# Kernel optimization log

Hardware: AMD Instinct MI355X
Metric: run time of the kernel (lower is better)

Reference implementation:

```python
import jax, jax.numpy as jnp
import numpy as np
from math import factorial

RS1 = [(16, 0), (8, 1), (4, 2)]
RS2 = [(16, 0), (8, 1), (4, 2)]


def _su2_cg(j1, j2, j3, m1, m2, m3):
    # Clebsch-Gordan coefficient <j1 m1 j2 m2 | j3 m3> (integer j's)
    if m3 != m1 + m2:
        return 0.0
    f = factorial
    vmin = int(max(-j1 + j2 + m3, -j1 + m1, 0))
    vmax = int(min(j2 + j3 + m1, j3 - j1 + j2, j3 + m3))
    C = ((2.0 * j3 + 1.0) * f(j3 + j1 - j2) * f(j3 - j1 + j2) * f(j1 + j2 - j3)
         * f(j3 + m3) * f(j3 - m3)
         / (f(j1 + j2 + j3 + 1) * f(j1 - m1) * f(j1 + m1) * f(j2 - m2) * f(j2 + m2))) ** 0.5
    S = 0.0
    for v in range(vmin, vmax + 1):
        S += (-1.0) ** (v + j2 + m2) * f(j2 + j3 + m1 - v) * f(j1 - m1 + v) \
             / (f(v) * f(j3 - j1 + j2 - v) * f(j3 + m3 - v) * f(v + j1 - j2 - m3))
    return C * S


def _su2_tensor(j1, j2, j3):
    C = np.zeros((2 * j1 + 1, 2 * j2 + 1, 2 * j3 + 1))
    for m1 in range(-j1, j1 + 1):
        for m2 in range(-j2, j2 + 1):
            m3 = m1 + m2
            if abs(m3) <= j3:
                C[m1 + j1, m2 + j2, m3 + j3] = _su2_cg(j1, j2, j3, m1, m2, m3)
    return C


def _change_basis_real_to_complex(l):
    q = np.zeros((2 * l + 1, 2 * l + 1), dtype=np.complex128)
    for m in range(-l, 0):
        q[l + m, l + abs(m)] = 2 ** -0.5
        q[l + m, l - abs(m)] = -1j * 2 ** -0.5
    q[l, l] = 1.0
    for m in range(1, l + 1):
        q[l + m, l + abs(m)] = (-1) ** m * 2 ** -0.5
        q[l + m, l - abs(m)] = 1j * (-1) ** m * 2 ** -0.5
    return ((-1j) ** l) * q


def _real_cg(l1, l2, l3):
    # CG tensor in the real spherical-harmonic basis, shape (2l1+1, 2l2+1, 2l3+1)
    C = _su2_tensor(l1, l2, l3)
    Q1 = _change_basis_real_to_complex(l1)
    Q2 = _change_basis_real_to_complex(l2)
    Q3 = _change_basis_real_to_complex(l3)
    C = np.einsum('ij,kl,mn,ikn->jlm', Q1, Q2, np.conj(Q3.T), C)
    return np.real(C)


def build_mixing_matrix(Rs1, Rs2):
    dim_in1 = sum(mul * (2 * l + 1) for mul, l in Rs1)
    dim_in2 = sum(mul * (2 * l + 1) for mul, l in Rs2)
    K = sum(m1 * m2 * (2 * l + 1)
            for m1, l1 in Rs1 for m2, l2 in Rs2
            for l in range(abs(l1 - l2), l1 + l2 + 1))
    M = np.zeros((K, dim_in1, dim_in2), dtype=np.float32)
    k_off = 0
    i_off = 0
    for mul1, l1 in Rs1:
        d1 = 2 * l1 + 1
        j_off = 0
        for mul2, l2 in Rs2:
            d2 = 2 * l2 + 1
            for l in range(abs(l1 - l2), l1 + l2 + 1):
                dl = 2 * l + 1
                # 'component' normalization
                C = (_real_cg(l1, l2, l) * (dl ** 0.5)).astype(np.float32)
                Ck = np.transpose(C, (2, 0, 1))  # (dl, d1, d2)
                for u in range(mul1):
                    for v in range(mul2):
                        k0 = k_off + (u * mul2 + v) * dl
                        M[k0:k0 + dl,
                          i_off + u * d1:i_off + (u + 1) * d1,
                          j_off + v * d2:j_off + (v + 1) * d2] = Ck
                k_off += mul1 * mul2 * dl
            j_off += mul2 * d2
        i_off += mul1 * d1
    return M


def setup_inputs() -> dict:
    key = jax.random.key(0)
    k1, k2 = jax.random.split(key)
    Z = 4096
    f1 = jax.random.normal(k1, (Z, 60), dtype=jnp.float32)
    f2 = jax.random.normal(k2, (Z, 60), dtype=jnp.float32)
    mix = jnp.asarray(build_mixing_matrix(RS1, RS2))  # (3600, 60, 60)
    return {"features_1": f1, "features_2": f2, "mixing_matrix": mix}


def reference(features_1, features_2, mixing_matrix):
    # output[z, k] = sum_{i,j} C[k,i,j] * f1[z,i] * f2[z,j]
    Z = features_1.shape[0]
    K, I, J = mixing_matrix.shape
    outer = jnp.einsum('zi,zj->zij', features_1, features_2).reshape(Z, I * J)
    return outer @ mixing_matrix.reshape(K, I * J).T
```

## Files before the change

### kernel.cpp

```cpp
#include <hip/hip_runtime.h>


#define ZT    32
#define ZPAD  36
#define NF    60
#define KTOT  3600
#define BLOCK 256

typedef float f32x4 __attribute__((ext_vector_type(4)));

struct Seg { short kstart, mul2, dl, d1, d2, ioff, joff; };

__constant__ Seg c_segs[20] = {
  {   0,16,1,1,1, 0, 0},
  { 256, 8,3,1,3, 0,16},
  { 640, 4,5,1,5, 0,40},
  { 960,16,3,3,1,16, 0},
  {1344, 8,1,3,3,16,16},
  {1408, 8,3,3,3,16,16},
  {1600, 8,5,3,3,16,16},
  {1920, 4,3,3,5,16,40},
  {2016, 4,5,3,5,16,40},
  {2176, 4,7,3,5,16,40},
  {2400,16,5,5,1,40, 0},
  {2720, 8,3,5,3,40,16},
  {2816, 8,5,5,3,40,16},
  {2976, 8,7,5,3,40,16},
  {3200, 4,1,5,5,40,40},
  {3216, 4,3,5,5,40,40},
  {3264, 4,5,5,5,40,40},
  {3344, 4,7,5,5,40,40},
  {3456, 4,9,5,5,40,40},
  {3600, 0,1,1,1, 0, 0}
};

template<int D1, int D2>
__device__ __forceinline__ void tp_body(const float* __restrict__ Crow,
    int i0, int j0,
    const float (&f1s)[NF][ZPAD], const float (&f2s)[NF][ZPAD],
    float* __restrict__ out, int k, int z0)
{
  float c[D1 * D2];
#pragma unroll
  for (int ii = 0; ii < D1; ++ii)
#pragma unroll
    for (int jj = 0; jj < D2; ++jj)
      c[ii * D2 + jj] = Crow[(i0 + ii) * NF + (j0 + jj)];

  float* op = out + (size_t)z0 * KTOT + k;

#pragma unroll 1
  for (int zz = 0; zz < ZT; zz += 4) {
    f32x4 a[D1], b[D2];
#pragma unroll
    for (int ii = 0; ii < D1; ++ii)
      a[ii] = *(const f32x4*)&f1s[i0 + ii][zz];
#pragma unroll
    for (int jj = 0; jj < D2; ++jj)
      b[jj] = *(const f32x4*)&f2s[j0 + jj][zz];

    float* opz = op + (size_t)zz * KTOT;
#pragma unroll
    for (int q = 0; q < 4; ++q) {
      float acc = 0.f;
      if constexpr (D1 <= D2) {
#pragma unroll
        for (int ii = 0; ii < D1; ++ii) {
          float t = 0.f;
#pragma unroll
          for (int jj = 0; jj < D2; ++jj)
            t = fmaf(c[ii * D2 + jj], b[jj][q], t);
          acc = fmaf(t, a[ii][q], acc);
        }
      } else {
#pragma unroll
        for (int jj = 0; jj < D2; ++jj) {
          float t = 0.f;
#pragma unroll
          for (int ii = 0; ii < D1; ++ii)
            t = fmaf(c[ii * D2 + jj], a[ii][q], t);
          acc = fmaf(t, b[jj][q], acc);
        }
      }
      opz[(size_t)q * KTOT] = acc;
    }
  }
}

__global__ __launch_bounds__(BLOCK) void tp_kernel(
    const float* __restrict__ f1, const float* __restrict__ f2,
    const float* __restrict__ M, float* __restrict__ out)
{
  __shared__ __align__(16) float f1s[NF][ZPAD];
  __shared__ __align__(16) float f2s[NF][ZPAD];
  const int z0 = blockIdx.y * ZT;

  {
    const float* f1p = f1 + (size_t)z0 * NF;
    const float* f2p = f2 + (size_t)z0 * NF;
    for (int t = threadIdx.x; t < (ZT * NF) / 4; t += BLOCK) {
      f32x4 v = *(const f32x4*)(f1p + t * 4);
      int zz = (t * 4) / NF;
      int f0 = (t * 4) % NF;
      f1s[f0 + 0][zz] = v[0]; f1s[f0 + 1][zz] = v[1];
      f1s[f0 + 2][zz] = v[2]; f1s[f0 + 3][zz] = v[3];
    }
    for (int t = threadIdx.x; t < (ZT * NF) / 4; t += BLOCK) {
      f32x4 v = *(const f32x4*)(f2p + t * 4);
      int zz = (t * 4) / NF;
      int f0 = (t * 4) % NF;
      f2s[f0 + 0][zz] = v[0]; f2s[f0 + 1][zz] = v[1];
      f2s[f0 + 2][zz] = v[2]; f2s[f0 + 3][zz] = v[3];
    }
  }
  __syncthreads();

  const int k = blockIdx.x * BLOCK + (int)threadIdx.x;
  if (k >= KTOT) return;

  int s = 0;
#pragma unroll 1
  while (k >= c_segs[s + 1].kstart) ++s;
  const Seg sg = c_segs[s];

  const int local = k - sg.kstart;
  const int uv = local / sg.dl;
  const int u  = uv / sg.mul2;
  const int v  = uv - u * sg.mul2;
  const int i0 = sg.ioff + u * sg.d1;
  const int j0 = sg.joff + v * sg.d2;
  const float* Crow = M + (size_t)k * (NF * NF);

  if (sg.d1 == 1) {
    if (sg.d2 == 1)      tp_body<1,1>(Crow, i0, j0, f1s, f2s, out, k, z0);
    else if (sg.d2 == 3) tp_body<1,3>(Crow, i0, j0, f1s, f2s, out, k, z0);
    else                 tp_body<1,5>(Crow, i0, j0, f1s, f2s, out, k, z0);
  } else if (sg.d1 == 3) {
    if (sg.d2 == 1)      tp_body<3,1>(Crow, i0, j0, f1s, f2s, out, k, z0);
    else if (sg.d2 == 3) tp_body<3,3>(Crow, i0, j0, f1s, f2s, out, k, z0);
    else                 tp_body<3,5>(Crow, i0, j0, f1s, f2s, out, k, z0);
  } else {
    if (sg.d2 == 1)      tp_body<5,1>(Crow, i0, j0, f1s, f2s, out, k, z0);
    else if (sg.d2 == 3) tp_body<5,3>(Crow, i0, j0, f1s, f2s, out, k, z0);
    else                 tp_body<5,5>(Crow, i0, j0, f1s, f2s, out, k, z0);
  }
}

extern "C" void kernel_launch(void* const* d_in, const int* in_sizes, int n_in,
                              void* d_out, int out_size, void* d_ws, size_t ws_size,
                              hipStream_t stream) {
  const float* f1 = (const float*)d_in[0];
  const float* f2 = (const float*)d_in[1];
  const float* M  = (const float*)d_in[2];
  float* out = (float*)d_out;

  const int Z = in_sizes[0] / NF;
  dim3 grid((KTOT + BLOCK - 1) / BLOCK,
            Z / ZT);
  tp_kernel<<<grid, dim3(BLOCK), 0, stream>>>(f1, f2, M, out);
}
```

Before: 27.58 us.

## Double-buffer LDS operand loads, overlap C and feature loads, double Z tile

Doubles the Z tile per block to 64, which halves the number of blocks and the grid-wide re-reads of the mixing rows. The global feature loads are issued into registers before the mixing coefficients are loaded and before the transposed LDS stores, so those latencies overlap. The segment lookup loop becomes a branchless compare-sum. The inner loop ping-pongs two register sets of shared-memory operands, and output writes use nontemporal stores. Costs are higher register pressure (launch bounds set to 3 blocks per CU), more LDS per block, and fewer blocks to spread across CUs.

```diff
diff --git a/kernel.cpp b/kernel.cpp
--- a/kernel.cpp
+++ b/kernel.cpp
@@ -1,148 +1,189 @@
 #include <hip/hip_runtime.h>
 
 
-#define ZT    32
-#define ZPAD  36
+#define ZT    64
+#define ZPAD  68
 #define NF    60
 #define KTOT  3600
 #define BLOCK 256
+#define NLD   ((ZT * NF) / 4)
 
 typedef float f32x4 __attribute__((ext_vector_type(4)));
 
-struct Seg { short kstart, mul2, dl, d1, d2, ioff, joff; };
-
-__constant__ Seg c_segs[20] = {
-  {   0,16,1,1,1, 0, 0},
-  { 256, 8,3,1,3, 0,16},
-  { 640, 4,5,1,5, 0,40},
-  { 960,16,3,3,1,16, 0},
-  {1344, 8,1,3,3,16,16},
-  {1408, 8,3,3,3,16,16},
-  {1600, 8,5,3,3,16,16},
-  {1920, 4,3,3,5,16,40},
-  {2016, 4,5,3,5,16,40},
-  {2176, 4,7,3,5,16,40},
-  {2400,16,5,5,1,40, 0},
-  {2720, 8,3,5,3,40,16},
-  {2816, 8,5,5,3,40,16},
-  {2976, 8,7,5,3,40,16},
-  {3200, 4,1,5,5,40,40},
-  {3216, 4,3,5,5,40,40},
-  {3264, 4,5,5,5,40,40},
-  {3344, 4,7,5,5,40,40},
-  {3456, 4,9,5,5,40,40},
-  {3600, 0,1,1,1, 0, 0}
+struct Seg { short kstart, mul2, dl, d1, d2, ioff, joff, pad; };
+
+__constant__ Seg c_segs[19] = {
+  {   0,16,1,1,1, 0, 0,0},
+  { 256, 8,3,1,3, 0,16,0},
+  { 640, 4,5,1,5, 0,40,0},
+  { 960,16,3,3,1,16, 0,0},
+  {1344, 8,1,3,3,16,16,0},
+  {1408, 8,3,3,3,16,16,0},
+  {1600, 8,5,3,3,16,16,0},
+  {1920, 4,3,3,5,16,40,0},
+  {2016, 4,5,3,5,16,40,0},
+  {2176, 4,7,3,5,16,40,0},
+  {2400,16,5,5,1,40, 0,0},
+  {2720, 8,3,5,3,40,16,0},
+  {2816, 8,5,5,3,40,16,0},
+  {2976, 8,7,5,3,40,16,0},
+  {3200, 4,1,5,5,40,40,0},
+  {3216, 4,3,5,5,40,40,0},
+  {3264, 4,5,5,5,40,40,0},
+  {3344, 4,7,5,5,40,40,0},
+  {3456, 4,9,5,5,40,40,0}
 };
 
 template<int D1, int D2>
-__device__ __forceinline__ void tp_body(const float* __restrict__ Crow,
-    int i0, int j0,
-    const float (&f1s)[NF][ZPAD], const float (&f2s)[NF][ZPAD],
-    float* __restrict__ out, int k, int z0)
-{
-  float c[D1 * D2];
+__device__ __forceinline__ void load_c(float (&c)[25],
+    const float* __restrict__ Crow, int i0, int j0)
+{
 #pragma unroll
   for (int ii = 0; ii < D1; ++ii)
 #pragma unroll
     for (int jj = 0; jj < D2; ++jj)
       c[ii * D2 + jj] = Crow[(i0 + ii) * NF + (j0 + jj)];
-
-  float* op = out + (size_t)z0 * KTOT + k;
-
+}
+
+template<int D1, int D2>
+__device__ __forceinline__ void ld_ab(f32x4 (&a)[D1], f32x4 (&b)[D2],
+    const float (&f1s)[NF][ZPAD], const float (&f2s)[NF][ZPAD],
+    int i0, int j0, int zz)
+{
+#pragma unroll
+  for (int ii = 0; ii < D1; ++ii) a[ii] = *(const f32x4*)&f1s[i0 + ii][zz];
+#pragma unroll
+  for (int jj = 0; jj < D2; ++jj) b[jj] = *(const f32x4*)&f2s[j0 + jj][zz];
+}
+
+template<int D1, int D2>
+__device__ __forceinline__ void comp_st(const float (&c)[25],
+    const f32x4 (&a)[D1], const f32x4 (&b)[D2], float* __restrict__ opz)
+{
+#pragma unroll
+  for (int q = 0; q < 4; ++q) {
+    float acc;
+    if constexpr (D1 <= D2) {
+      acc = 0.f;
+#pragma unroll
+      for (int ii = 0; ii < D1; ++ii) {
+        float t = c[ii * D2] * b[0][q];
+#pragma unroll
+        for (int jj = 1; jj < D2; ++jj) t = fmaf(c[ii * D2 + jj], b[jj][q], t);
+        acc = fmaf(t, a[ii][q], acc);
+      }
+    } else {
+      acc = 0.f;
+#pragma unroll
+      for (int jj = 0; jj < D2; ++jj) {
+        float t = c[jj] * a[0][q];
+#pragma unroll
+        for (int ii = 1; ii < D1; ++ii) t = fmaf(c[ii * D2 + jj], a[ii][q], t);
+        acc = fmaf(t, b[jj][q], acc);
+      }
+    }
+    __builtin_nontemporal_store(acc, opz + (size_t)q * KTOT);
+  }
+}
+
+template<int D1, int D2>
+__device__ void tp_body(const float (&c)[25], int i0, int j0,
+    const float (&f1s)[NF][ZPAD], const float (&f2s)[NF][ZPAD],
+    float* __restrict__ op)
+{
+  f32x4 aA[D1], bA[D2], aB[D1], bB[D2];
+  ld_ab<D1,D2>(aA, bA, f1s, f2s, i0, j0, 0);
 #pragma unroll 1
-  for (int zz = 0; zz < ZT; zz += 4) {
-    f32x4 a[D1], b[D2];
-#pragma unroll
-    for (int ii = 0; ii < D1; ++ii)
-      a[ii] = *(const f32x4*)&f1s[i0 + ii][zz];
-#pragma unroll
-    for (int jj = 0; jj < D2; ++jj)
-      b[jj] = *(const f32x4*)&f2s[j0 + jj][zz];
-
-    float* opz = op + (size_t)zz * KTOT;
-#pragma unroll
-    for (int q = 0; q < 4; ++q) {
-      float acc = 0.f;
-      if constexpr (D1 <= D2) {
-#pragma unroll
-        for (int ii = 0; ii < D1; ++ii) {
-          float t = 0.f;
-#pragma unroll
-          for (int jj = 0; jj < D2; ++jj)
-            t = fmaf(c[ii * D2 + jj], b[jj][q], t);
-          acc = fmaf(t, a[ii][q], acc);
-        }
-      } else {
-#pragma unroll
-        for (int jj = 0; jj < D2; ++jj) {
-          float t = 0.f;
-#pragma unroll
-          for (int ii = 0; ii < D1; ++ii)
-            t = fmaf(c[ii * D2 + jj], a[ii][q], t);
-          acc = fmaf(t, b[jj][q], acc);
-        }
-      }
-      opz[(size_t)q * KTOT] = acc;
-    }
-  }
-}
-
-__global__ __launch_bounds__(BLOCK) void tp_kernel(
+  for (int zz = 0; zz < ZT; zz += 8) {
+    ld_ab<D1,D2>(aB, bB, f1s, f2s, i0, j0, zz + 4);
+    comp_st<D1,D2>(c, aA, bA, op + (size_t)zz * KTOT);
+    if (zz + 8 < ZT) ld_ab<D1,D2>(aA, bA, f1s, f2s, i0, j0, zz + 8);
+    comp_st<D1,D2>(c, aB, bB, op + (size_t)(zz + 4) * KTOT);
+  }
+}
+
+__global__ __launch_bounds__(BLOCK, 3) void tp_kernel(
     const float* __restrict__ f1, const float* __restrict__ f2,
     const float* __restrict__ M, float* __restrict__ out)
 {
   __shared__ __align__(16) float f1s[NF][ZPAD];
   __shared__ __align__(16) float f2s[NF][ZPAD];
-  const int z0 = blockIdx.y * ZT;
-
-  {
-    const float* f1p = f1 + (size_t)z0 * NF;
-    const float* f2p = f2 + (size_t)z0 * NF;
-    for (int t = threadIdx.x; t < (ZT * NF) / 4; t += BLOCK) {
-      f32x4 v = *(const f32x4*)(f1p + t * 4);
-      int zz = (t * 4) / NF;
-      int f0 = (t * 4) % NF;
-      f1s[f0 + 0][zz] = v[0]; f1s[f0 + 1][zz] = v[1];
-      f1s[f0 + 2][zz] = v[2]; f1s[f0 + 3][zz] = v[3];
+  const int z0  = blockIdx.y * ZT;
+  const int tid = (int)threadIdx.x;
+
+  const float* f1p = f1 + (size_t)z0 * NF;
+  const float* f2p = f2 + (size_t)z0 * NF;
+  f32x4 s1[4], s2[4];
+#pragma unroll
+  for (int r = 0; r < 4; ++r) {
+    int t = tid + r * BLOCK;
+    if (t < NLD) {
+      s1[r] = *(const f32x4*)(f1p + t * 4);
+      s2[r] = *(const f32x4*)(f2p + t * 4);
     }
-    for (int t = threadIdx.x; t < (ZT * NF) / 4; t += BLOCK) {
-      f32x4 v = *(const f32x4*)(f2p + t * 4);
-      int zz = (t * 4) / NF;
-      int f0 = (t * 4) % NF;
-      f2s[f0 + 0][zz] = v[0]; f2s[f0 + 1][zz] = v[1];
-      f2s[f0 + 2][zz] = v[2]; f2s[f0 + 3][zz] = v[3];
-    }
-  }
-  __syncthreads();
-
-  const int k = blockIdx.x * BLOCK + (int)threadIdx.x;
-  if (k >= KTOT) return;
-
+  }
+
+  const int k  = blockIdx.x * BLOCK + tid;
+  const int kc = k < KTOT ? k : KTOT - 1;
   int s = 0;
-#pragma unroll 1
-  while (k >= c_segs[s + 1].kstart) ++s;
+  s += (kc >=  256); s += (kc >=  640); s += (kc >=  960); s += (kc >= 1344);
+  s += (kc >= 1408); s += (kc >= 1600); s += (kc >= 1920); s += (kc >= 2016);
+  s += (kc >= 2176); s += (kc >= 2400); s += (kc >= 2720); s += (kc >= 2816);
+  s += (kc >= 2976); s += (kc >= 3200); s += (kc >= 3216); s += (kc >= 3264);
+  s += (kc >= 3344); s += (kc >= 3456);
   const Seg sg = c_segs[s];
-
-  const int local = k - sg.kstart;
+  const int local = kc - sg.kstart;
   const int uv = local / sg.dl;
   const int u  = uv / sg.mul2;
   const int v  = uv - u * sg.mul2;
   const int i0 = sg.ioff + u * sg.d1;
   const int j0 = sg.joff + v * sg.d2;
-  const float* Crow = M + (size_t)k * (NF * NF);
-
-  if (sg.d1 == 1) {
-    if (sg.d2 == 1)      tp_body<1,1>(Crow, i0, j0, f1s, f2s, out, k, z0);
-    else if (sg.d2 == 3) tp_body<1,3>(Crow, i0, j0, f1s, f2s, out, k, z0);
-    else                 tp_body<1,5>(Crow, i0, j0, f1s, f2s, out, k, z0);
-  } else if (sg.d1 == 3) {
-    if (sg.d2 == 1)      tp_body<3,1>(Crow, i0, j0, f1s, f2s, out, k, z0);
-    else if (sg.d2 == 3) tp_body<3,3>(Crow, i0, j0, f1s, f2s, out, k, z0);
-    else                 tp_body<3,5>(Crow, i0, j0, f1s, f2s, out, k, z0);
+  const float* Crow = M + (size_t)kc * (NF * NF);
+
+  float c[25];
+  const int d1 = sg.d1, d2 = sg.d2;
+  if (d1 == 1) {
+    if (d2 == 1)      load_c<1,1>(c, Crow, i0, j0);
+    else if (d2 == 3) load_c<1,3>(c, Crow, i0, j0);
+    else              load_c<1,5>(c, Crow, i0, j0);
+  } else if (d1 == 3) {
+    if (d2 == 1)      load_c<3,1>(c, Crow, i0, j0);
+    else if (d2 == 3) load_c<3,3>(c, Crow, i0, j0);
+    else              load_c<3,5>(c, Crow, i0, j0);
   } else {
-    if (sg.d2 == 1)      tp_body<5,1>(Crow, i0, j0, f1s, f2s, out, k, z0);
-    else if (sg.d2 == 3) tp_body<5,3>(Crow, i0, j0, f1s, f2s, out, k, z0);
-    else                 tp_body<5,5>(Crow, i0, j0, f1s, f2s, out, k, z0);
+    if (d2 == 1)      load_c<5,1>(c, Crow, i0, j0);
+    else if (d2 == 3) load_c<5,3>(c, Crow, i0, j0);
+    else              load_c<5,5>(c, Crow, i0, j0);
+  }
+
+#pragma unroll
+  for (int r = 0; r < 4; ++r) {
+    int t = tid + r * BLOCK;
+    if (t < NLD) {
+      int g = t * 4, zz = g / NF, f0 = g % NF;
+      f1s[f0 + 0][zz] = s1[r][0]; f1s[f0 + 1][zz] = s1[r][1];
+      f1s[f0 + 2][zz] = s1[r][2]; f1s[f0 + 3][zz] = s1[r][3];
+      f2s[f0 + 0][zz] = s2[r][0]; f2s[f0 + 1][zz] = s2[r][1];
+      f2s[f0 + 2][zz] = s2[r][2]; f2s[f0 + 3][zz] = s2[r][3];
+    }
+  }
+  __syncthreads();
+
+  if (k >= KTOT) return;
+  float* op = out + (size_t)z0 * KTOT + k;
+
+  if (d1 == 1) {
+    if (d2 == 1)      tp_body<1,1>(c, i0, j0, f1s, f2s, op);
+    else if (d2 == 3) tp_body<1,3>(c, i0, j0, f1s, f2s, op);
+    else              tp_body<1,5>(c, i0, j0, f1s, f2s, op);
+  } else if (d1 == 3) {
+    if (d2 == 1)      tp_body<3,1>(c, i0, j0, f1s, f2s, op);
+    else if (d2 == 3) tp_body<3,3>(c, i0, j0, f1s, f2s, op);
+    else              tp_body<3,5>(c, i0, j0, f1s, f2s, op);
+  } else {
+    if (d2 == 1)      tp_body<5,1>(c, i0, j0, f1s, f2s, op);
+    else if (d2 == 3) tp_body<5,3>(c, i0, j0, f1s, f2s, op);
+    else              tp_body<5,5>(c, i0, j0, f1s, f2s, op);
   }
 }
 
```

New measurement: 25.61 us. 1.08x faster.
